# Kernel optimization log

Hardware: AMD Instinct MI355X
Metric: run time of the kernel (lower is better)

## Reference

```python
import jax, jax.numpy as jnp
import numpy as np
import math

H, D, DFF = 12, 768, 3072
DH = D // H  # 64
B, T = 4, 2048
EPS = 1e-5


def setup_inputs() -> dict:
    key = jax.random.key(0)
    ks = jax.random.split(key, 12)
    randw = lambda k, *d: jax.random.normal(k, d, jnp.float32) / math.sqrt(d[-1])
    return {
        "X": jax.random.normal(ks[0], (B, T, D), jnp.float32),
        "w_q": randw(ks[1], H, DH, D),
        "w_k": randw(ks[2], H, DH, D),
        "w_v": randw(ks[3], H, DH, D),
        "w_o": randw(ks[4], DH * H, D),
        "W1": jax.random.normal(ks[5], (DFF, D), jnp.float32) * 0.02,
        "b1": jnp.zeros((DFF,), jnp.float32),
        "W2": jax.random.normal(ks[6], (D, DFF), jnp.float32) * 0.02,
        "b2": jnp.zeros((D,), jnp.float32),
        "g1": jnp.ones((D,), jnp.float32),
        "be1": jnp.zeros((D,), jnp.float32),
        "g2": jnp.ones((D,), jnp.float32),
        "be2": jnp.zeros((D,), jnp.float32),
    }


def layernorm(x, g, b):
    mu = jnp.mean(x, axis=-1, keepdims=True)
    var = jnp.var(x, axis=-1, keepdims=True)
    return (x - mu) * jax.lax.rsqrt(var + EPS) * g + b


def attention(x, w_q, w_k, w_v, w_o):
    # x: [n,t,c]
    q = jnp.einsum('ntc,hdc->nhtd', x, w_q)
    k = jnp.einsum('ntc,hdc->nhtd', x, w_k)
    v = jnp.einsum('ntc,hdc->nhtd', x, w_v)
    a = jnp.einsum('nhtd,nhsd->nhts', q, k) / math.sqrt(q.shape[3])
    t, s = a.shape[2], a.shape[3]
    forbidden = jnp.arange(t)[:, None] < jnp.arange(s)[None, :]
    a = jnp.where(forbidden, -jnp.inf, a)
    a = jax.nn.softmax(a, axis=3)
    y = jnp.einsum('nhts,nhsd->nthd', a, v).reshape(x.shape[0], t, -1)
    return y @ w_o


def reference(X, w_q, w_k, w_v, w_o, W1, b1, W2, b2, g1, be1, g2, be2):
    X = X + attention(layernorm(X, g1, be1), w_q, w_k, w_v, w_o)
    h = jax.nn.relu(layernorm(X, g2, be2) @ W1.T + b1)
    return X + h @ W2.T + b2
```

## Files before the change

kernel.cpp:

```cpp
#include <hip/hip_runtime.h>
#include <stdint.h>

#define B_   4
#define T_   2048
#define D_   768
#define H_   12
#define DH_  64
#define DFF_ 3072
#define NTOK_ (B_*T_)
#define QKVN_ (3*D_)

typedef unsigned short u16;
typedef unsigned int u32;
typedef __bf16 bf16x8 __attribute__((ext_vector_type(8)));
typedef float  f32x4  __attribute__((ext_vector_type(4)));

__device__ __forceinline__ u16 f2bf(float f) {
  union { float f; unsigned u; } v; v.f = f;
  return (u16)((v.u + 0x7fffu + ((v.u >> 16) & 1u)) >> 16);
}

__device__ __forceinline__ float fast_exp2(float x) {
#if __has_builtin(__builtin_amdgcn_exp2f)
  return __builtin_amdgcn_exp2f(x);
#else
  return exp2f(x);
#endif
}

__device__ __forceinline__ float fast_rcp(float x) {
#if __has_builtin(__builtin_amdgcn_rcpf)
  return __builtin_amdgcn_rcpf(x);
#else
  return 1.0f / x;
#endif
}

__device__ __forceinline__ void gload_lds16(const void* g, void* l) {
  __builtin_amdgcn_global_load_lds(
      (__attribute__((address_space(1))) unsigned int*)(void*)g,
      (__attribute__((address_space(3))) unsigned int*)l, 16, 0, 0);
}

template<bool BIAS, bool RELU, bool RES, bool BF16OUT, bool QSCALE, int BN,
         bool VTRANS>
__global__ __launch_bounds__(256) void gemm_bt(
    const u16* __restrict__ A, const u16* __restrict__ Bw,
    const float* __restrict__ bias, const float* __restrict__ res,
    void* __restrict__ outp, u16* __restrict__ vtp, int M, int N, int K)
{
  constexpr int NI = BN / 32;
  __shared__ u16 lA[2 * 128 * 32];
  __shared__ u16 lB[2 * BN * 32];
  const int tid  = threadIdx.x;
  const int lane = tid & 63;
  const int wave = tid >> 6;
  const int quad = lane >> 4;
  const int l15  = lane & 15;
  const int mBase = blockIdx.x * 128;
  const int nBase = blockIdx.y * BN;
  const int wm = (wave >> 1) * 64;
  const int wn = (wave & 1) * (BN / 2);

  const f32x4 fz = {0.f, 0.f, 0.f, 0.f};
  f32x4 acc[4][NI];
#pragma unroll
  for (int i = 0; i < 4; i++)
#pragma unroll
    for (int j = 0; j < NI; j++) acc[i][j] = fz;

  const int c0 = tid, c1 = tid + 256;
  const int ra0 = c0 >> 2, ja0 = (c0 & 3) ^ ((ra0 >> 1) & 3);
  const int ra1 = c1 >> 2, ja1 = (c1 & 3) ^ ((ra1 >> 1) & 3);
  const u16* gA0 = A  + (size_t)(mBase + ra0) * K + ja0 * 8;
  const u16* gA1 = A  + (size_t)(mBase + ra1) * K + ja1 * 8;
  const u16* gB0 = Bw + (size_t)(nBase + ra0) * K + ja0 * 8;
  const u16* gB1 = (BN == 128)
      ? Bw + (size_t)(nBase + ra1) * K + ja1 * 8 : nullptr;
  u16* lA0 = lA + c0 * 8; u16* lA1 = lA + c1 * 8;
  u16* lB0 = lB + c0 * 8;
  u16* lB1 = (BN == 128) ? lB + c1 * 8 : nullptr;

  const int ca = (quad ^ ((l15 >> 1) & 3)) * 8;

  for (int kt = 0; kt < K; kt += 64) {
    gload_lds16(gA0 + kt,      lA0);
    gload_lds16(gA1 + kt,      lA1);
    gload_lds16(gA0 + kt + 32, lA0 + 128 * 32);
    gload_lds16(gA1 + kt + 32, lA1 + 128 * 32);
    gload_lds16(gB0 + kt,      lB0);
    gload_lds16(gB0 + kt + 32, lB0 + BN * 32);
    if (BN == 128) {
      gload_lds16(gB1 + kt,      lB1);
      gload_lds16(gB1 + kt + 32, lB1 + BN * 32);
    }
    __syncthreads();
#pragma unroll
    for (int hf = 0; hf < 2; hf++) {
      const u16* lAh = lA + hf * (128 * 32);
      const u16* lBh = lB + hf * (BN * 32);
      bf16x8 af[4], bfr[NI];
#pragma unroll
      for (int mi = 0; mi < 4; mi++)
        af[mi] = *(const bf16x8*)(lAh + (wm + mi * 16 + l15) * 32 + ca);
#pragma unroll
      for (int ni = 0; ni < NI; ni++)
        bfr[ni] = *(const bf16x8*)(lBh + (wn + ni * 16 + l15) * 32 + ca);
#pragma unroll
      for (int mi = 0; mi < 4; mi++)
#pragma unroll
        for (int ni = 0; ni < NI; ni++)
          acc[mi][ni] = __builtin_amdgcn_mfma_f32_16x16x32_bf16(
              af[mi], bfr[ni], acc[mi][ni], 0, 0, 0);
    }
    __syncthreads();
  }

#pragma unroll
  for (int mi = 0; mi < 4; mi++) {
#pragma unroll
    for (int ni = 0; ni < NI; ni++) {
      const int col = nBase + wn + ni * 16 + l15;
      if (VTRANS && col >= 2 * D_) {
        const int n  = col - 2 * D_;
        const int hh = n >> 6, dd = n & 63;
        const int row0 = mBase + wm + mi * 16 + quad * 4;
        const int bb = row0 >> 11, tt = row0 & (T_ - 1);
        const int tperm = (tt & ~31) + 8 * quad + 4 * (mi & 1);
        ushort4 pk;
        pk.x = f2bf(acc[mi][ni][0]); pk.y = f2bf(acc[mi][ni][1]);
        pk.z = f2bf(acc[mi][ni][2]); pk.w = f2bf(acc[mi][ni][3]);
        *(ushort4*)(vtp + ((size_t)((bb * H_ + hh) * DH_ + dd)) * T_ + tperm) = pk;
        continue;
      }
      float bv = 0.f;
      if (BIAS) bv = bias[col];
#pragma unroll
      for (int r = 0; r < 4; r++) {
        const int row = mBase + wm + mi * 16 + quad * 4 + r;
        float v = acc[mi][ni][r];
        if (BIAS) v += bv;
        if (RELU) v = fmaxf(v, 0.f);
        if (RES)  v += res[(size_t)row * N + col];
        if (QSCALE && col < D_) v *= 0.180336880f;
        if (BF16OUT) ((u16*)outp)[(size_t)row * N + col] = f2bf(v);
        else        ((float*)outp)[(size_t)row * N + col] = v;
      }
    }
  }
}

__device__ __forceinline__ void attn_round(
    const u16* __restrict__ lKc, const u16* __restrict__ lVc,
    int s0, int qw0, int quad, int l15,
    int kc0, int kc1,
    const bf16x8& q0, const bf16x8& q1,
    f32x4 (&o)[4], float& ls)
{
  const f32x4 fz = {0.f, 0.f, 0.f, 0.f};
  f32x4 s[4];
#pragma unroll
  for (int ni = 0; ni < 4; ni++) {
    const int rb = (ni * 16 + l15) * 64;
    const bf16x8 k0 = *(const bf16x8*)(lKc + rb + kc0);
    const bf16x8 k1 = *(const bf16x8*)(lKc + rb + kc1);
    f32x4 t = fz;
    t = __builtin_amdgcn_mfma_f32_16x16x32_bf16(k0, q0, t, 0, 0, 0);
    t = __builtin_amdgcn_mfma_f32_16x16x32_bf16(k1, q1, t, 0, 0, 0);
    s[ni] = t;
  }

  const bool nm = (s0 + 63 > qw0);
  union { __bf16 h[16]; bf16x8 v[2]; } P;
  float ls0 = 0.f, ls1 = 0.f;
  if (nm) {
    const int qidx = qw0 + l15;
#pragma unroll
    for (int ni = 0; ni < 4; ni++) {
      const int sbase = s0 + ni * 16 + quad * 4;
#pragma unroll
      for (int r = 0; r < 4; r++) {
        float v = fast_exp2(s[ni][r]);
        if (sbase + r > qidx) v = 0.f;
        P.h[ni * 4 + r] = (__bf16)v;
        if (r & 1) ls1 += v; else ls0 += v;
      }
    }
  } else {
#pragma unroll
    for (int ni = 0; ni < 4; ni++) {
#pragma unroll
      for (int r = 0; r < 4; r++) {
        float v = fast_exp2(s[ni][r]);
        P.h[ni * 4 + r] = (__bf16)v;
        if (r & 1) ls1 += v; else ls0 += v;
      }
    }
  }
  ls += ls0 + ls1;

#pragma unroll
  for (int dt = 0; dt < 4; dt++) {
    const int rb = (dt * 16 + l15) * 64;
    const bf16x8 v0 = *(const bf16x8*)(lVc + rb + kc0);
    const bf16x8 v1 = *(const bf16x8*)(lVc + rb + kc1);
    o[dt] = __builtin_amdgcn_mfma_f32_16x16x32_bf16(v0, P.v[0], o[dt], 0, 0, 0);
    o[dt] = __builtin_amdgcn_mfma_f32_16x16x32_bf16(v1, P.v[1], o[dt], 0, 0, 0);
  }
}

__global__ __launch_bounds__(256) void attn_kernel(
    const u16* __restrict__ qkv, const u16* __restrict__ vt, u16* __restrict__ Y)
{
  __shared__ u16 lK[2][64 * 64];
  __shared__ u16 lV[2][64 * 64];
  const int tid  = threadIdx.x;
  const int lane = tid & 63;
  const int wave = tid >> 6;
  const int quad = lane >> 4;
  const int l15  = lane & 15;
  const int pi = (int)blockIdx.x;
  const int h  = blockIdx.y;
  const int b  = blockIdx.z;
  const int tH = 31 - pi, tL = pi;
  const int njsH = tH + 1;
  const int total = njsH + tL + 1;
  const int qwH = tH * 64 + wave * 16;
  const int qwL = tL * 64 + wave * 16;

  const int sw  = l15 & 7;
  const int kc0 = (quad ^ sw) * 8;
  const int kc1 = ((4 + quad) ^ sw) * 8;

  bf16x8 qH0, qH1, qL0, qL1;
  {
    const u16* qp = qkv + (size_t)(b * T_ + qwH + l15) * QKVN_ + h * DH_ + quad * 8;
    qH0 = *(const bf16x8*)(qp);
    qH1 = *(const bf16x8*)(qp + 32);
    const u16* qp2 = qkv + (size_t)(b * T_ + qwL + l15) * QKVN_ + h * DH_ + quad * 8;
    qL0 = *(const bf16x8*)(qp2);
    qL1 = *(const bf16x8*)(qp2 + 32);
  }

  const f32x4 fz = {0.f, 0.f, 0.f, 0.f};
  f32x4 oH[4], oL[4];
#pragma unroll
  for (int i = 0; i < 4; i++) { oH[i] = fz; oL[i] = fz; }
  float lsH = 0.f, lsL = 0.f;

  const int c0 = tid, c1 = tid + 256;
  const int r0 = c0 >> 3, j0 = (c0 & 7) ^ (r0 & 7);
  const int r1 = c1 >> 3, j1 = (c1 & 7) ^ (r1 & 7);
  const u16* gK0 = qkv + (size_t)(b * T_ + r0) * QKVN_ + D_ + h * DH_ + j0 * 8;
  const u16* gK1 = qkv + (size_t)(b * T_ + r1) * QKVN_ + D_ + h * DH_ + j1 * 8;
  const u16* gV0 = vt + (size_t)((b * H_ + h) * DH_ + r0) * T_ + j0 * 8;
  const u16* gV1 = vt + (size_t)((b * H_ + h) * DH_ + r1) * T_ + j1 * 8;

  gload_lds16(gK0, lK[0] + c0 * 8);
  gload_lds16(gK1, lK[0] + c1 * 8);
  gload_lds16(gV0, lV[0] + c0 * 8);
  gload_lds16(gV1, lV[0] + c1 * 8);

  for (int i = 0; i < total; i++) {
    const int cur = i & 1;
    __syncthreads();

    if (i + 1 < total) {
      const int sn = (i + 1 < njsH) ? (i + 1) : (i + 1 - njsH);
      const size_t s1 = (size_t)sn * 64;
      const int nb = cur ^ 1;
      gload_lds16(gK0 + s1 * QKVN_, lK[nb] + c0 * 8);
      gload_lds16(gK1 + s1 * QKVN_, lK[nb] + c1 * 8);
      gload_lds16(gV0 + s1,         lV[nb] + c0 * 8);
      gload_lds16(gV1 + s1,         lV[nb] + c1 * 8);
    }

    const u16* lKc = lK[cur];
    const u16* lVc = lV[cur];
    if (i < njsH) {
      attn_round(lKc, lVc, i * 64, qwH, quad, l15, kc0, kc1,
                 qH0, qH1, oH, lsH);
    } else {
      attn_round(lKc, lVc, (i - njsH) * 64, qwL, quad, l15, kc0, kc1,
                 qL0, qL1, oL, lsL);
    }
  }

  lsH += __shfl_xor(lsH, 16); lsH += __shfl_xor(lsH, 32);
  lsL += __shfl_xor(lsL, 16); lsL += __shfl_xor(lsL, 32);
  const float rlH = fast_rcp(lsH);
  const float rlL = fast_rcp(lsL);

#pragma unroll
  for (int dt = 0; dt < 4; dt++) {
    const int dbase = h * DH_ + dt * 16 + quad * 4;
    ushort4 pa, pb;
    pa.x = f2bf(oH[dt][0] * rlH); pa.y = f2bf(oH[dt][1] * rlH);
    pa.z = f2bf(oH[dt][2] * rlH); pa.w = f2bf(oH[dt][3] * rlH);
    pb.x = f2bf(oL[dt][0] * rlL); pb.y = f2bf(oL[dt][1] * rlL);
    pb.z = f2bf(oL[dt][2] * rlL); pb.w = f2bf(oL[dt][3] * rlL);
    *(ushort4*)(Y + (size_t)(b * T_ + qwH + l15) * D_ + dbase) = pa;
    *(ushort4*)(Y + (size_t)(b * T_ + qwL + l15) * D_ + dbase) = pb;
  }
}

__device__ __forceinline__ void ln_row(
    const float* __restrict__ X, const float* __restrict__ g,
    const float* __restrict__ be, u16* __restrict__ out, int row)
{
  const float* x = X + (size_t)row * D_;
  const int t = threadIdx.x;
  const float v0 = x[t], v1 = x[t + 256], v2 = x[t + 512];
  float s = v0 + v1 + v2;
  float sq = v0 * v0 + v1 * v1 + v2 * v2;
#pragma unroll
  for (int off = 1; off < 64; off <<= 1) {
    s  += __shfl_xor(s, off);
    sq += __shfl_xor(sq, off);
  }
  __shared__ float ws_[4], wq_[4];
  const int wv = t >> 6, lane = t & 63;
  if (lane == 0) { ws_[wv] = s; wq_[wv] = sq; }
  __syncthreads();
  s  = ws_[0] + ws_[1] + ws_[2] + ws_[3];
  sq = wq_[0] + wq_[1] + wq_[2] + wq_[3];
  const float mean = s * (1.f / 768.f);
  const float var  = sq * (1.f / 768.f) - mean * mean;
  const float rstd = rsqrtf(var + 1e-5f);
  u16* o = out + (size_t)row * D_;
  int c = t;
  o[c] = f2bf((v0 - mean) * rstd * g[c] + be[c]); c += 256;
  o[c] = f2bf((v1 - mean) * rstd * g[c] + be[c]); c += 256;
  o[c] = f2bf((v2 - mean) * rstd * g[c] + be[c]);
}

__global__ __launch_bounds__(256) void ln_kernel(
    const float* __restrict__ X, const float* __restrict__ g,
    const float* __restrict__ be, u16* __restrict__ out)
{
  ln_row(X, g, be, out, blockIdx.x);
}

__global__ __launch_bounds__(256) void prep_kernel(
    const float* __restrict__ X, const float* __restrict__ g1,
    const float* __restrict__ be1, u16* __restrict__ xln,
    const float* __restrict__ w_q, const float* __restrict__ w_k,
    const float* __restrict__ w_v, const float* __restrict__ W1,
    const float* __restrict__ W2, const float* __restrict__ w_o,
    u16* __restrict__ wqkv, u16* __restrict__ W1b,
    u16* __restrict__ W2b, u16* __restrict__ woT)
{
  if (blockIdx.x < NTOK_) {
    ln_row(X, g1, be1, xln, blockIdx.x);
    return;
  }
  const int id = blockIdx.x - NTOK_;
  if (id < 144) {
    __shared__ float tile[64][65];
    const int bx = id % 12, by = id / 12;
    const int rr0 = by * 64, cc0 = bx * 64;
    for (int idx = threadIdx.x; idx < 4096; idx += 256) {
      const int i = idx >> 6, j = idx & 63;
      tile[i][j] = w_o[(size_t)(rr0 + i) * D_ + cc0 + j];
    }
    __syncthreads();
    for (int idx = threadIdx.x; idx < 4096; idx += 256) {
      const int i = idx >> 6, j = idx & 63;
      woT[(size_t)(cc0 + i) * D_ + rr0 + j] = f2bf(tile[j][i]);
    }
  } else {
    const int WQN = H_ * DH_ * D_;
    const int i = (id - 144) * 256 + threadIdx.x;
    if (i < 3 * WQN) {
      const float* src = (i < WQN) ? w_q : (i < 2 * WQN ? w_k : w_v);
      const int off = (i < WQN) ? i : (i < 2 * WQN ? i - WQN : i - 2 * WQN);
      wqkv[i] = f2bf(src[off]);
    } else if (i < 3 * WQN + DFF_ * D_) {
      const int off = i - 3 * WQN;
      W1b[off] = f2bf(W1[off]);
    } else {
      const int off = i - 3 * WQN - DFF_ * D_;
      W2b[off] = f2bf(W2[off]);
    }
  }
}

extern "C" void kernel_launch(void* const* d_in, const int* in_sizes, int n_in,
                              void* d_out, int out_size, void* d_ws, size_t ws_size,
                              hipStream_t stream) {
  const float* X   = (const float*)d_in[0];
  const float* w_q = (const float*)d_in[1];
  const float* w_k = (const float*)d_in[2];
  const float* w_v = (const float*)d_in[3];
  const float* w_o = (const float*)d_in[4];
  const float* W1  = (const float*)d_in[5];
  const float* b1  = (const float*)d_in[6];
  const float* W2  = (const float*)d_in[7];
  const float* b2  = (const float*)d_in[8];
  const float* g1  = (const float*)d_in[9];
  const float* be1 = (const float*)d_in[10];
  const float* g2  = (const float*)d_in[11];
  const float* be2 = (const float*)d_in[12];
  float* out = (float*)d_out;

  char* ws = (char*)d_ws;
  u16*   qkv  = (u16*)(ws + 0);
  u16*   vt   = (u16*)(ws + 37748736);
  u16*   hbuf = (u16*)(ws + 0);
  u16*   xln  = (u16*)(ws + 50331648);
  u16*   Ybuf = (u16*)(ws + 62914560);
  float* X1   = (float*)(ws + 75497472);
  u16*   wqkv = (u16*)(ws + 100663296);
  u16*   woT  = (u16*)(ws + 104202240);
  u16*   W1b  = (u16*)(ws + 105381888);
  u16*   W2b  = (u16*)(ws + 110100480);

  prep_kernel<<<NTOK_ + 25488, 256, 0, stream>>>(
      X, g1, be1, xln, w_q, w_k, w_v, W1, W2, w_o, wqkv, W1b, W2b, woT);

  gemm_bt<false, false, false, true, true, 128, true>
      <<<dim3(64, 18), 256, 0, stream>>>(
      xln, wqkv, nullptr, nullptr, qkv, vt, NTOK_, QKVN_, D_);

  attn_kernel<<<dim3(16, 12, 4), 256, 0, stream>>>(qkv, vt, Ybuf);

  gemm_bt<false, false, true, false, false, 64, false>
      <<<dim3(64, 12), 256, 0, stream>>>(
      Ybuf, woT, nullptr, X, X1, nullptr, NTOK_, D_, D_);

  ln_kernel<<<NTOK_, 256, 0, stream>>>(X1, g2, be2, xln);

  gemm_bt<true, true, false, true, false, 128, false>
      <<<dim3(64, 24), 256, 0, stream>>>(
      xln, W1b, b1, nullptr, hbuf, nullptr, NTOK_, DFF_, D_);

  gemm_bt<true, false, true, false, false, 64, false>
      <<<dim3(64, 12), 256, 0, stream>>>(
      hbuf, W2b, b2, X1, out, nullptr, NTOK_, D_, DFF_);
}
```

Measured before the change: 348.7 us.

## Double-buffer GEMM LDS tiles to overlap next K-slice loads with MFMA

Restructures the GEMM main loop from a single 64-wide K step (load both halves, sync, compute, sync) into a ping-pong pipeline over 32-wide K slices. The next slice is prefetched into the alternate LDS buffer while the current one feeds the MFMAs, so global-to-LDS latency can hide behind compute. The cost is twice as many loop iterations and barriers per K, and there is only one barrier per step with the async loads' completion relying on that barrier.

```diff
diff --git a/kernel.cpp b/kernel.cpp
--- a/kernel.cpp
+++ b/kernel.cpp
@@ -50,8 +50,8 @@
     void* __restrict__ outp, u16* __restrict__ vtp, int M, int N, int K)
 {
   constexpr int NI = BN / 32;
-  __shared__ u16 lA[2 * 128 * 32];
-  __shared__ u16 lB[2 * BN * 32];
+  __shared__ u16 lA[2][128 * 32];
+  __shared__ u16 lB[2][BN * 32];
   const int tid  = threadIdx.x;
   const int lane = tid & 63;
   const int wave = tid >> 6;
@@ -77,42 +77,42 @@
   const u16* gB0 = Bw + (size_t)(nBase + ra0) * K + ja0 * 8;
   const u16* gB1 = (BN == 128)
       ? Bw + (size_t)(nBase + ra1) * K + ja1 * 8 : nullptr;
-  u16* lA0 = lA + c0 * 8; u16* lA1 = lA + c1 * 8;
-  u16* lB0 = lB + c0 * 8;
-  u16* lB1 = (BN == 128) ? lB + c1 * 8 : nullptr;
 
   const int ca = (quad ^ ((l15 >> 1) & 3)) * 8;
 
-  for (int kt = 0; kt < K; kt += 64) {
-    gload_lds16(gA0 + kt,      lA0);
-    gload_lds16(gA1 + kt,      lA1);
-    gload_lds16(gA0 + kt + 32, lA0 + 128 * 32);
-    gload_lds16(gA1 + kt + 32, lA1 + 128 * 32);
-    gload_lds16(gB0 + kt,      lB0);
-    gload_lds16(gB0 + kt + 32, lB0 + BN * 32);
-    if (BN == 128) {
-      gload_lds16(gB1 + kt,      lB1);
-      gload_lds16(gB1 + kt + 32, lB1 + BN * 32);
-    }
-    __syncthreads();
-#pragma unroll
-    for (int hf = 0; hf < 2; hf++) {
-      const u16* lAh = lA + hf * (128 * 32);
-      const u16* lBh = lB + hf * (BN * 32);
-      bf16x8 af[4], bfr[NI];
-#pragma unroll
-      for (int mi = 0; mi < 4; mi++)
-        af[mi] = *(const bf16x8*)(lAh + (wm + mi * 16 + l15) * 32 + ca);
+  const int nk = K >> 5;
+  gload_lds16(gA0, lA[0] + c0 * 8);
+  gload_lds16(gA1, lA[0] + c1 * 8);
+  gload_lds16(gB0, lB[0] + c0 * 8);
+  if (BN == 128) gload_lds16(gB1, lB[0] + c1 * 8);
+  __syncthreads();
+
+  for (int t = 0; t < nk; t++) {
+    const int cur = t & 1;
+    if (t + 1 < nk) {
+      const int kof = (t + 1) * 32;
+      u16* dA = lA[cur ^ 1];
+      u16* dB = lB[cur ^ 1];
+      gload_lds16(gA0 + kof, dA + c0 * 8);
+      gload_lds16(gA1 + kof, dA + c1 * 8);
+      gload_lds16(gB0 + kof, dB + c0 * 8);
+      if (BN == 128) gload_lds16(gB1 + kof, dB + c1 * 8);
+    }
+    const u16* lAh = lA[cur];
+    const u16* lBh = lB[cur];
+    bf16x8 af[4], bfr[NI];
+#pragma unroll
+    for (int mi = 0; mi < 4; mi++)
+      af[mi] = *(const bf16x8*)(lAh + (wm + mi * 16 + l15) * 32 + ca);
+#pragma unroll
+    for (int ni = 0; ni < NI; ni++)
+      bfr[ni] = *(const bf16x8*)(lBh + (wn + ni * 16 + l15) * 32 + ca);
+#pragma unroll
+    for (int mi = 0; mi < 4; mi++)
 #pragma unroll
       for (int ni = 0; ni < NI; ni++)
-        bfr[ni] = *(const bf16x8*)(lBh + (wn + ni * 16 + l15) * 32 + ca);
-#pragma unroll
-      for (int mi = 0; mi < 4; mi++)
-#pragma unroll
-        for (int ni = 0; ni < NI; ni++)
-          acc[mi][ni] = __builtin_amdgcn_mfma_f32_16x16x32_bf16(
-              af[mi], bfr[ni], acc[mi][ni], 0, 0, 0);
-    }
+        acc[mi][ni] = __builtin_amdgcn_mfma_f32_16x16x32_bf16(
+            af[mi], bfr[ni], acc[mi][ni], 0, 0, 0);
     __syncthreads();
   }
 
```

Result: slower. 362.6 us (+4.0%).
